# Performance work log

Hardware: AMD Instinct MI355X
Metric: run time of the kernel (lower is better)

The kernel has to match this reference:

```python
import jax, jax.numpy as jnp
import numpy as np

N_NODES = 50000
N_EDGES = 800000
NODE_DIM = 64
EDGE_DIM = 32
OUT_FEATS = 64


def setup_inputs() -> dict:
    key = jax.random.key(0)
    k1, k2, k3, k4, k5, k6, k7 = jax.random.split(key, 7)
    node_features = jax.random.normal(k1, (N_NODES, NODE_DIM), dtype=jnp.float32)
    edge_features = jax.random.normal(k2, (N_EDGES, EDGE_DIM), dtype=jnp.float32)
    src = jax.random.randint(k3, (N_EDGES,), 0, N_NODES, dtype=jnp.int32)
    dst = jax.random.randint(k4, (N_EDGES,), 0, N_NODES, dtype=jnp.int32)
    in_dim = 2 * NODE_DIM + EDGE_DIM  # concat([e_ft, h_src, h_dst])
    w_group = jax.random.normal(k5, (in_dim,), dtype=jnp.float32) * 0.05
    w_srcattn = jax.random.normal(k6, (NODE_DIM + EDGE_DIM,), dtype=jnp.float32) * 0.05
    w_lin = jax.random.normal(k7, (in_dim, OUT_FEATS), dtype=jnp.float32) * 0.05
    return {"node_features": node_features, "edge_features": edge_features,
            "src": src, "dst": dst,
            "w_group": w_group, "w_srcattn": w_srcattn, "w_lin": w_lin}


def _segment_softmax(scores, seg, num_segments):
    # numerically-stable softmax of per-edge scalar scores within each segment
    m = jax.ops.segment_max(scores, seg, num_segments=num_segments)
    e = jnp.exp(scores - m[seg])
    s = jax.ops.segment_sum(e, seg, num_segments=num_segments)
    return e / s[seg]


def reference(node_features, edge_features, src, dst, w_group, w_srcattn, w_lin):
    h = node_features              # [N, node_dim]
    e_ft = edge_features           # [E, edge_dim]
    h_src = h[src]                 # [E, node_dim]
    h_dst = h[dst]                 # [E, node_dim]

    # --- group_apply_edges(group_by='src'): edge attention over out-edges of each src ---
    z2 = jnp.concatenate([e_ft, h_src, h_dst], axis=1)      # [E, edge_dim + 2*node_dim]
    a = z2 @ w_group                                        # [E]
    gamma = _segment_softmax(a, src, N_NODES)               # softmax over edges sharing src
    e_weighted = gamma[:, None] * e_ft                      # [E, edge_dim]

    # --- gnn_msg: msg = concat([h_src, e_weighted]) ---
    msg = jnp.concatenate([h_src, e_weighted], axis=1)      # [E, node_dim + edge_dim]

    # --- gnn_reduce: attention softmax over mailbox (edges sharing dst), weighted sum ---
    s = msg @ w_srcattn                                     # [E]
    alpha = _segment_softmax(s, dst, N_NODES)
    accum = jax.ops.segment_sum(alpha[:, None] * msg, dst, num_segments=N_NODES)  # [N, node_dim+edge_dim]

    # --- node_update: linear(concat([h, accum])) + relu ---
    h_cat = jnp.concatenate([h, accum], axis=1)             # [N, 2*node_dim + edge_dim]
    out = jax.nn.relu(h_cat @ w_lin)                        # [N, out_feats]
    return out
```

## Files before the change

### kernel.cpp

```cpp
#include <hip/hip_runtime.h>

#define NN 50000
#define NE 800000
#define NEB 1563
#define NHB 3125
#define NTILES 3125

typedef __attribute__((ext_vector_type(8))) short bf16x8;
typedef __attribute__((ext_vector_type(4))) short s16x4;
typedef __attribute__((ext_vector_type(4))) float f32x4;
typedef __attribute__((ext_vector_type(4))) int   i32x4;

static __device__ __forceinline__ short f2bf(float f) {
    unsigned int u = __float_as_uint(f);
    u += 0x7FFFu + ((u >> 16) & 1u);
    return (short)(u >> 16);
}

__global__ __launch_bounds__(256) void k_pre(
    const float* __restrict__ h, const int* __restrict__ dst,
    const float* __restrict__ wg, const float* __restrict__ wa,
    int* __restrict__ cnt, int* __restrict__ rank,
    float* __restrict__ p1, float* __restrict__ pd, float* __restrict__ dpf,
    short* __restrict__ hb)
{
    int tid = threadIdx.x;
    if (blockIdx.x < NEB) {
        int e0 = blockIdx.x * 512 + tid;
        if (e0 >= NE) return;
        int e1 = e0 + 256;
        bool v1 = e1 < NE;
        int d0 = dst[e0];
        int d1 = dst[v1 ? e1 : 0];
        int r0 = atomicAdd(&cnt[d0], 1);
        int r1 = v1 ? atomicAdd(&cnt[d1], 1) : 0;
        rank[e0] = r0;
        if (v1) rank[e1] = r1;
        return;
    }
    __shared__ float4 ls[16], ld[16], lt[16];
    if (tid < 16)      ls[tid]      = ((const float4*)wg)[8 + tid];
    else if (tid < 32) ld[tid - 16] = ((const float4*)wg)[8 + tid];
    else if (tid < 48) lt[tid - 32] = ((const float4*)wa)[tid - 32];
    __syncthreads();
    int n = (blockIdx.x - NEB) * 16 + (tid >> 4);
    if (n >= NN) return;
    int l16 = tid & 15;
    float4 v = ((const float4*)(h + (size_t)n * 64))[l16];
    s16x4 hv;
    hv[0] = f2bf(v.x); hv[1] = f2bf(v.y); hv[2] = f2bf(v.z); hv[3] = f2bf(v.w);
    *(s16x4*)(hb + (size_t)n * 160 + l16 * 4) = hv;
    float4 w1 = ls[l16], w2 = ld[l16], w3 = lt[l16];
    float s1 = v.x*w1.x + v.y*w1.y + v.z*w1.z + v.w*w1.w;
    float s2 = v.x*w2.x + v.y*w2.y + v.z*w2.z + v.w*w2.w;
    float s3 = v.x*w3.x + v.y*w3.y + v.z*w3.z + v.w*w3.w;
    #pragma unroll
    for (int m = 8; m; m >>= 1) {
        s1 += __shfl_xor(s1, m);
        s2 += __shfl_xor(s2, m);
        s3 += __shfl_xor(s3, m);
    }
    if (l16 == 0) { p1[n] = s1; pd[n] = s2; dpf[2 * n + 1] = s3; }
}

__global__ __launch_bounds__(256) void k_assign(
    const int* __restrict__ cnt, int* __restrict__ off, int* __restrict__ gtotal)
{
    int n = blockIdx.x * 256 + threadIdx.x;
    int lane = threadIdx.x & 63;
    int c = (n < NN) ? cnt[n] : 0;
    int pre = c;
    #pragma unroll
    for (int d = 1; d < 64; d <<= 1) {
        int v = __shfl_up(pre, d);
        if (lane >= d) pre += v;
    }
    int base = 0;
    if (lane == 63) base = atomicAdd(gtotal, pre);
    base = __shfl(base, 63);
    if (n < NN) off[n] = base + pre - c;
}

__global__ __launch_bounds__(256) void k_edge(
    const float* __restrict__ ef, const int* __restrict__ src,
    const int* __restrict__ dst, const int* __restrict__ rank,
    const float* __restrict__ wg, const float* __restrict__ wa,
    const float* __restrict__ p1, const float* __restrict__ pd,
    float* __restrict__ dpf, const int* __restrict__ off,
    i32x4* __restrict__ recA)
{
    __shared__ float4 lwe[8], lae[8];
    int tid = threadIdx.x;
    if (tid < 8)       lwe[tid]     = ((const float4*)wg)[tid];
    else if (tid < 16) lae[tid - 8] = ((const float4*)wa)[tid - 8 + 16];
    __syncthreads();
    int e0 = blockIdx.x * 512 + tid;
    if (e0 >= NE) return;
    int e1 = e0 + 256;
    bool v1 = e1 < NE;
    int e1c = v1 ? e1 : 0;
    int s0 = src[e0], d0 = dst[e0], k0 = rank[e0];
    int s1 = src[e1c], d1 = dst[e1c], k1 = rank[e1c];
    float p1a = p1[s0], pda = pd[d0];
    float p1b = p1[s1], pdb = pd[d1];
    int o0 = off[d0], o1 = off[d1];
    const float4* ea = (const float4*)ef + (unsigned)e0 * 8u;
    const float4* eb = (const float4*)ef + (unsigned)e1c * 8u;
    float a0 = 0.f, u0 = 0.f, a1 = 0.f, u1 = 0.f;
    #pragma unroll
    for (int q = 0; q < 8; ++q) {
        float4 x = ea[q], y = eb[q];
        float4 w = lwe[q], w2 = lae[q];
        a0 += x.x*w.x  + x.y*w.y  + x.z*w.z  + x.w*w.w;
        u0 += x.x*w2.x + x.y*w2.y + x.z*w2.z + x.w*w2.w;
        a1 += y.x*w.x  + y.y*w.y  + y.z*w.z  + y.w*w.w;
        u1 += y.x*w2.x + y.y*w2.y + y.z*w2.z + y.w*w2.w;
    }
    float ev0 = __expf(a0 + p1a + pda);
    float ev1 = __expf(a1 + p1b + pdb);
    atomicAdd(&dpf[2 * s0], ev0);
    if (v1) atomicAdd(&dpf[2 * s1], ev1);
    i32x4 rc0 = (i32x4){s0, e0, __float_as_int(ev0), __float_as_int(u0)};
    __builtin_nontemporal_store(rc0, recA + (o0 + k0));
    if (v1) {
        i32x4 rc1 = (i32x4){s1, e1, __float_as_int(ev1), __float_as_int(u1)};
        __builtin_nontemporal_store(rc1, recA + (o1 + k1));
    }
}

__global__ __launch_bounds__(256) void k_reduce(
    const float* __restrict__ h, const float* __restrict__ ef,
    const int* __restrict__ cnt, const int* __restrict__ off,
    const float2* __restrict__ dp, const i32x4* __restrict__ recA,
    short* __restrict__ hb)
{
    int n = blockIdx.x * 4 + (threadIdx.x >> 6);
    if (n >= NN) return;
    int lane = threadIdx.x & 63;
    bool up = lane >= 32;
    int l5 = lane & 31;
    int deg = cnt[n], base = off[n];
    const i32x4* rp = recA + base;
    float acch = 0.f, acce = 0.f, den = 0.f;
    int j = 0;
    for (; j + 8 <= deg; j += 8) {
        i32x4 r[8];
        #pragma unroll
        for (int t = 0; t < 8; ++t) r[t] = rp[j + t];
        float2 dv[8];
        #pragma unroll
        for (int t = 0; t < 8; ++t) dv[t] = dp[r[t][0]];
        float hv[8];
        #pragma unroll
        for (int t = 0; t < 8; ++t) hv[t] = h[((unsigned)r[t][0] << 6) + lane];
        float efv[4];
        #pragma unroll
        for (int t = 0; t < 4; ++t) {
            int e = up ? r[2*t+1][1] : r[2*t][1];
            efv[t] = ef[((unsigned)e << 5) + l5];
        }
        float g[8], s[8];
        #pragma unroll
        for (int t = 0; t < 8; ++t) {
            g[t] = __int_as_float(r[t][2]) * __builtin_amdgcn_rcpf(dv[t].x);
            s[t] = __expf(dv[t].y + g[t] * __int_as_float(r[t][3]));
            den  += s[t];
            acch += s[t] * hv[t];
        }
        #pragma unroll
        for (int t = 0; t < 4; ++t) {
            float w = up ? s[2*t+1]*g[2*t+1] : s[2*t]*g[2*t];
            acce += w * efv[t];
        }
    }
    if (j + 4 <= deg) {
        i32x4 r[4];
        #pragma unroll
        for (int t = 0; t < 4; ++t) r[t] = rp[j + t];
        float2 dv[4];
        #pragma unroll
        for (int t = 0; t < 4; ++t) dv[t] = dp[r[t][0]];
        float hv[4];
        #pragma unroll
        for (int t = 0; t < 4; ++t) hv[t] = h[((unsigned)r[t][0] << 6) + lane];
        float efv[2];
        #pragma unroll
        for (int t = 0; t < 2; ++t) {
            int e = up ? r[2*t+1][1] : r[2*t][1];
            efv[t] = ef[((unsigned)e << 5) + l5];
        }
        float g[4], s[4];
        #pragma unroll
        for (int t = 0; t < 4; ++t) {
            g[t] = __int_as_float(r[t][2]) * __builtin_amdgcn_rcpf(dv[t].x);
            s[t] = __expf(dv[t].y + g[t] * __int_as_float(r[t][3]));
            den  += s[t];
            acch += s[t] * hv[t];
        }
        #pragma unroll
        for (int t = 0; t < 2; ++t) {
            float w = up ? s[2*t+1]*g[2*t+1] : s[2*t]*g[2*t];
            acce += w * efv[t];
        }
        j += 4;
    }
    for (; j < deg; ++j) {
        i32x4 r = rp[j];
        float2 dt = dp[r[0]];
        float g = __int_as_float(r[2]) * __builtin_amdgcn_rcpf(dt.x);
        float s = __expf(dt.y + g * __int_as_float(r[3]));
        den += s;
        acch += s * h[((unsigned)r[0] << 6) + lane];
        if (!up) acce += s * g * ef[((unsigned)r[1] << 5) + l5];
    }
    acce += __shfl_xor(acce, 32);
    float inv = (deg > 0) ? __builtin_amdgcn_rcpf(den) : 0.f;
    size_t hbase = (size_t)n * 160;
    hb[hbase + 64 + lane] = f2bf(acch * inv);
    if (!up) hb[hbase + 128 + l5] = f2bf(acce * inv);
}

__global__ __launch_bounds__(256) void k_node_update(
    const short* __restrict__ hb, const float* __restrict__ wl_g,
    float* __restrict__ out)
{
    int lane = threadIdx.x & 63;
    int col  = lane & 15;
    int quad = lane >> 4;
    int tile = blockIdx.x * 4 + (threadIdx.x >> 6);
    if (tile >= NTILES) return;

    bf16x8 bfr[5][4];
    #pragma unroll
    for (int kc = 0; kc < 5; ++kc)
        #pragma unroll
        for (int nt = 0; nt < 4; ++nt) {
            #pragma unroll
            for (int j = 0; j < 8; ++j) {
                int k = kc * 32 + quad * 8 + j;
                bfr[kc][nt][j] = f2bf(wl_g[k * 64 + nt * 16 + col]);
            }
        }

    int n = tile * 16 + col;
    f32x4 acc[4];
    #pragma unroll
    for (int nt = 0; nt < 4; ++nt) acc[nt] = (f32x4){0.f, 0.f, 0.f, 0.f};

    const short* hrow = hb + (size_t)n * 160 + quad * 8;
    #pragma unroll
    for (int kc = 0; kc < 5; ++kc) {
        bf16x8 af = *(const bf16x8*)(hrow + kc * 32);
        #pragma unroll
        for (int nt = 0; nt < 4; ++nt)
            acc[nt] = __builtin_amdgcn_mfma_f32_16x16x32_bf16(
                af, bfr[kc][nt], acc[nt], 0, 0, 0);
    }

    #pragma unroll
    for (int nt = 0; nt < 4; ++nt) {
        #pragma unroll
        for (int r = 0; r < 4; ++r) {
            int node = tile * 16 + quad * 4 + r;
            out[(size_t)node * 64 + nt * 16 + col] = fmaxf(acc[nt][r], 0.f);
        }
    }
}

extern "C" void kernel_launch(void* const* d_in, const int* in_sizes, int n_in,
                              void* d_out, int out_size, void* d_ws, size_t ws_size,
                              hipStream_t stream)
{
    const float* h   = (const float*)d_in[0];
    const float* ef  = (const float*)d_in[1];
    const int*   src = (const int*)d_in[2];
    const int*   dst = (const int*)d_in[3];
    const float* wg  = (const float*)d_in[4];
    const float* wa  = (const float*)d_in[5];
    const float* wl  = (const float*)d_in[6];
    float* out = (float*)d_out;

    float* ws = (float*)d_ws;
    float*  dpf    = ws;
    int*    cnt    = (int*)(ws + 2 * NN);
    int*    gtotal = (int*)(ws + 3 * NN);
    int*    off    = (int*)(ws + 3 * NN + 16);
    float*  p1     = ws + 4 * NN + 16;
    float*  pd     = ws + 5 * NN + 16;
    i32x4*  recA   = (i32x4*)(ws + 6 * NN + 16);
    int*    rank   = (int*)(ws + 6 * NN + 16 + 4 * NE);
    short*  hb     = (short*)(ws + 6 * NN + 16 + 5 * NE);

    hipMemsetAsync(d_ws, 0, (size_t)(3 * NN + 16) * sizeof(float), stream);

    k_pre<<<NEB + NHB, 256, 0, stream>>>(h, dst, wg, wa, cnt, rank, p1, pd, dpf, hb);
    k_assign<<<(NN + 255) / 256, 256, 0, stream>>>(cnt, off, gtotal);
    k_edge<<<NEB, 256, 0, stream>>>(ef, src, dst, rank, wg, wa, p1, pd, dpf,
                                    off, recA);
    k_reduce<<<(NN + 3) / 4, 256, 0, stream>>>(h, ef, cnt, off, (const float2*)dpf,
                                               recA, hb);
    k_node_update<<<782, 256, 0, stream>>>(hb, wl, out);
}
```

Before: 356.3 us.

## Replace scattered 16B edge records with int index list plus per-edge float2 data

The edge kernel now writes a coalesced per-edge float2 (exp score, attention projection) indexed by edge id, and scatters only a 4-byte edge index into the dst-sorted list instead of a 16-byte record. The reduce kernel gathers src and recB through that index, which adds an extra level of indirection. The histogram and node projection are split into separate kernels, each edge thread handles one edge, and pd and off are packed into one int2 array. The aim is to cut scattered write traffic in the edge pass, at the cost of more dependent random reads in the reduce pass.

```diff
diff --git a/kernel.cpp b/kernel.cpp
--- a/kernel.cpp
+++ b/kernel.cpp
@@ -2,14 +2,13 @@
 
 #define NN 50000
 #define NE 800000
-#define NEB 1563
+#define NEB 3125
 #define NHB 3125
 #define NTILES 3125
 
 typedef __attribute__((ext_vector_type(8))) short bf16x8;
 typedef __attribute__((ext_vector_type(4))) short s16x4;
 typedef __attribute__((ext_vector_type(4))) float f32x4;
-typedef __attribute__((ext_vector_type(4))) int   i32x4;
 
 static __device__ __forceinline__ short f2bf(float f) {
     unsigned int u = __float_as_uint(f);
@@ -17,33 +16,25 @@
     return (short)(u >> 16);
 }
 
-__global__ __launch_bounds__(256) void k_pre(
-    const float* __restrict__ h, const int* __restrict__ dst,
-    const float* __restrict__ wg, const float* __restrict__ wa,
-    int* __restrict__ cnt, int* __restrict__ rank,
-    float* __restrict__ p1, float* __restrict__ pd, float* __restrict__ dpf,
-    short* __restrict__ hb)
-{
+__global__ __launch_bounds__(256) void k_hist(
+    const int* __restrict__ dst, int* __restrict__ cnt, int* __restrict__ rank)
+{
+    int e = blockIdx.x * 256 + threadIdx.x;
+    if (e < NE) rank[e] = atomicAdd(&cnt[dst[e]], 1);
+}
+
+__global__ __launch_bounds__(256) void k_proj(
+    const float* __restrict__ h, const float* __restrict__ wg,
+    const float* __restrict__ wa, float* __restrict__ p1,
+    int2* __restrict__ pdo, float* __restrict__ dpf, short* __restrict__ hb)
+{
+    __shared__ float4 ls[16], ld[16], lt[16];
     int tid = threadIdx.x;
-    if (blockIdx.x < NEB) {
-        int e0 = blockIdx.x * 512 + tid;
-        if (e0 >= NE) return;
-        int e1 = e0 + 256;
-        bool v1 = e1 < NE;
-        int d0 = dst[e0];
-        int d1 = dst[v1 ? e1 : 0];
-        int r0 = atomicAdd(&cnt[d0], 1);
-        int r1 = v1 ? atomicAdd(&cnt[d1], 1) : 0;
-        rank[e0] = r0;
-        if (v1) rank[e1] = r1;
-        return;
-    }
-    __shared__ float4 ls[16], ld[16], lt[16];
     if (tid < 16)      ls[tid]      = ((const float4*)wg)[8 + tid];
     else if (tid < 32) ld[tid - 16] = ((const float4*)wg)[8 + tid];
     else if (tid < 48) lt[tid - 32] = ((const float4*)wa)[tid - 32];
     __syncthreads();
-    int n = (blockIdx.x - NEB) * 16 + (tid >> 4);
+    int n = blockIdx.x * 16 + (tid >> 4);
     if (n >= NN) return;
     int l16 = tid & 15;
     float4 v = ((const float4*)(h + (size_t)n * 64))[l16];
@@ -60,11 +51,15 @@
         s2 += __shfl_xor(s2, m);
         s3 += __shfl_xor(s3, m);
     }
-    if (l16 == 0) { p1[n] = s1; pd[n] = s2; dpf[2 * n + 1] = s3; }
+    if (l16 == 0) {
+        p1[n] = s1;
+        pdo[n].x = __float_as_int(s2);
+        dpf[2 * n + 1] = s3;
+    }
 }
 
 __global__ __launch_bounds__(256) void k_assign(
-    const int* __restrict__ cnt, int* __restrict__ off, int* __restrict__ gtotal)
+    const int* __restrict__ cnt, int2* __restrict__ pdo, int* __restrict__ gtotal)
 {
     int n = blockIdx.x * 256 + threadIdx.x;
     int lane = threadIdx.x & 63;
@@ -78,60 +73,48 @@
     int base = 0;
     if (lane == 63) base = atomicAdd(gtotal, pre);
     base = __shfl(base, 63);
-    if (n < NN) off[n] = base + pre - c;
+    if (n < NN) pdo[n].y = base + pre - c;
 }
 
 __global__ __launch_bounds__(256) void k_edge(
     const float* __restrict__ ef, const int* __restrict__ src,
     const int* __restrict__ dst, const int* __restrict__ rank,
     const float* __restrict__ wg, const float* __restrict__ wa,
-    const float* __restrict__ p1, const float* __restrict__ pd,
-    float* __restrict__ dpf, const int* __restrict__ off,
-    i32x4* __restrict__ recA)
+    const float* __restrict__ p1, const int2* __restrict__ pdo,
+    float* __restrict__ dpf, int* __restrict__ eidx,
+    float2* __restrict__ recB)
 {
     __shared__ float4 lwe[8], lae[8];
     int tid = threadIdx.x;
     if (tid < 8)       lwe[tid]     = ((const float4*)wg)[tid];
     else if (tid < 16) lae[tid - 8] = ((const float4*)wa)[tid - 8 + 16];
     __syncthreads();
-    int e0 = blockIdx.x * 512 + tid;
-    if (e0 >= NE) return;
-    int e1 = e0 + 256;
-    bool v1 = e1 < NE;
-    int e1c = v1 ? e1 : 0;
-    int s0 = src[e0], d0 = dst[e0], k0 = rank[e0];
-    int s1 = src[e1c], d1 = dst[e1c], k1 = rank[e1c];
-    float p1a = p1[s0], pda = pd[d0];
-    float p1b = p1[s1], pdb = pd[d1];
-    int o0 = off[d0], o1 = off[d1];
-    const float4* ea = (const float4*)ef + (unsigned)e0 * 8u;
-    const float4* eb = (const float4*)ef + (unsigned)e1c * 8u;
-    float a0 = 0.f, u0 = 0.f, a1 = 0.f, u1 = 0.f;
+    int e = blockIdx.x * 256 + tid;
+    if (e >= NE) return;
+    int s = src[e], d = dst[e], rk = rank[e];
+    float p1v = p1[s];
+    int2 pv = pdo[d];
+    float pdv = __int_as_float(pv.x);
+    int pos = pv.y + rk;
+    const float4* e4 = (const float4*)(ef + (size_t)e * 32);
+    float a = 0.f, u = 0.f;
     #pragma unroll
     for (int q = 0; q < 8; ++q) {
-        float4 x = ea[q], y = eb[q];
-        float4 w = lwe[q], w2 = lae[q];
-        a0 += x.x*w.x  + x.y*w.y  + x.z*w.z  + x.w*w.w;
-        u0 += x.x*w2.x + x.y*w2.y + x.z*w2.z + x.w*w2.w;
-        a1 += y.x*w.x  + y.y*w.y  + y.z*w.z  + y.w*w.w;
-        u1 += y.x*w2.x + y.y*w2.y + y.z*w2.z + y.w*w2.w;
-    }
-    float ev0 = __expf(a0 + p1a + pda);
-    float ev1 = __expf(a1 + p1b + pdb);
-    atomicAdd(&dpf[2 * s0], ev0);
-    if (v1) atomicAdd(&dpf[2 * s1], ev1);
-    i32x4 rc0 = (i32x4){s0, e0, __float_as_int(ev0), __float_as_int(u0)};
-    __builtin_nontemporal_store(rc0, recA + (o0 + k0));
-    if (v1) {
-        i32x4 rc1 = (i32x4){s1, e1, __float_as_int(ev1), __float_as_int(u1)};
-        __builtin_nontemporal_store(rc1, recA + (o1 + k1));
-    }
+        float4 v = e4[q], w = lwe[q], w2 = lae[q];
+        a += v.x*w.x  + v.y*w.y  + v.z*w.z  + v.w*w.w;
+        u += v.x*w2.x + v.y*w2.y + v.z*w2.z + v.w*w2.w;
+    }
+    float ev = __expf(a + p1v + pdv);
+    atomicAdd(&dpf[2 * s], ev);
+    recB[e] = make_float2(ev, u);
+    eidx[pos] = e;
 }
 
 __global__ __launch_bounds__(256) void k_reduce(
     const float* __restrict__ h, const float* __restrict__ ef,
-    const int* __restrict__ cnt, const int* __restrict__ off,
-    const float2* __restrict__ dp, const i32x4* __restrict__ recA,
+    const int* __restrict__ src, const int* __restrict__ cnt,
+    const int2* __restrict__ pdo, const float2* __restrict__ dp,
+    const int* __restrict__ eidx, const float2* __restrict__ recB,
     short* __restrict__ hb)
 {
     int n = blockIdx.x * 4 + (threadIdx.x >> 6);
@@ -139,31 +122,34 @@
     int lane = threadIdx.x & 63;
     bool up = lane >= 32;
     int l5 = lane & 31;
-    int deg = cnt[n], base = off[n];
-    const i32x4* rp = recA + base;
+    int deg = cnt[n], base = pdo[n].y;
+    const int* ep = eidx + base;
     float acch = 0.f, acce = 0.f, den = 0.f;
     int j = 0;
     for (; j + 8 <= deg; j += 8) {
-        i32x4 r[8];
-        #pragma unroll
-        for (int t = 0; t < 8; ++t) r[t] = rp[j + t];
-        float2 dv[8];
-        #pragma unroll
-        for (int t = 0; t < 8; ++t) dv[t] = dp[r[t][0]];
-        float hv[8];
-        #pragma unroll
-        for (int t = 0; t < 8; ++t) hv[t] = h[((unsigned)r[t][0] << 6) + lane];
+        int e[8];
+        #pragma unroll
+        for (int t = 0; t < 8; ++t) e[t] = ep[j + t];
+        float2 rb[8]; int sv[8];
+        #pragma unroll
+        for (int t = 0; t < 8; ++t) { rb[t] = recB[e[t]]; sv[t] = src[e[t]]; }
+        float2 dv[8]; float hv[8];
+        #pragma unroll
+        for (int t = 0; t < 8; ++t) {
+            dv[t] = dp[sv[t]];
+            hv[t] = h[((unsigned)sv[t] << 6) + lane];
+        }
         float efv[4];
         #pragma unroll
         for (int t = 0; t < 4; ++t) {
-            int e = up ? r[2*t+1][1] : r[2*t][1];
-            efv[t] = ef[((unsigned)e << 5) + l5];
+            int ee = up ? e[2*t+1] : e[2*t];
+            efv[t] = ef[((unsigned)ee << 5) + l5];
         }
         float g[8], s[8];
         #pragma unroll
         for (int t = 0; t < 8; ++t) {
-            g[t] = __int_as_float(r[t][2]) * __builtin_amdgcn_rcpf(dv[t].x);
-            s[t] = __expf(dv[t].y + g[t] * __int_as_float(r[t][3]));
+            g[t] = rb[t].x * __builtin_amdgcn_rcpf(dv[t].x);
+            s[t] = __expf(dv[t].y + g[t] * rb[t].y);
             den  += s[t];
             acch += s[t] * hv[t];
         }
@@ -174,26 +160,29 @@
         }
     }
     if (j + 4 <= deg) {
-        i32x4 r[4];
-        #pragma unroll
-        for (int t = 0; t < 4; ++t) r[t] = rp[j + t];
-        float2 dv[4];
-        #pragma unroll
-        for (int t = 0; t < 4; ++t) dv[t] = dp[r[t][0]];
-        float hv[4];
-        #pragma unroll
-        for (int t = 0; t < 4; ++t) hv[t] = h[((unsigned)r[t][0] << 6) + lane];
+        int e[4];
+        #pragma unroll
+        for (int t = 0; t < 4; ++t) e[t] = ep[j + t];
+        float2 rb[4]; int sv[4];
+        #pragma unroll
+        for (int t = 0; t < 4; ++t) { rb[t] = recB[e[t]]; sv[t] = src[e[t]]; }
+        float2 dv[4]; float hv[4];
+        #pragma unroll
+        for (int t = 0; t < 4; ++t) {
+            dv[t] = dp[sv[t]];
+            hv[t] = h[((unsigned)sv[t] << 6) + lane];
+        }
         float efv[2];
         #pragma unroll
         for (int t = 0; t < 2; ++t) {
-            int e = up ? r[2*t+1][1] : r[2*t][1];
-            efv[t] = ef[((unsigned)e << 5) + l5];
+            int ee = up ? e[2*t+1] : e[2*t];
+            efv[t] = ef[((unsigned)ee << 5) + l5];
         }
         float g[4], s[4];
         #pragma unroll
         for (int t = 0; t < 4; ++t) {
-            g[t] = __int_as_float(r[t][2]) * __builtin_amdgcn_rcpf(dv[t].x);
-            s[t] = __expf(dv[t].y + g[t] * __int_as_float(r[t][3]));
+            g[t] = rb[t].x * __builtin_amdgcn_rcpf(dv[t].x);
+            s[t] = __expf(dv[t].y + g[t] * rb[t].y);
             den  += s[t];
             acch += s[t] * hv[t];
         }
@@ -205,13 +194,15 @@
         j += 4;
     }
     for (; j < deg; ++j) {
-        i32x4 r = rp[j];
-        float2 dt = dp[r[0]];
-        float g = __int_as_float(r[2]) * __builtin_amdgcn_rcpf(dt.x);
-        float s = __expf(dt.y + g * __int_as_float(r[3]));
-        den += s;
-        acch += s * h[((unsigned)r[0] << 6) + lane];
-        if (!up) acce += s * g * ef[((unsigned)r[1] << 5) + l5];
+        int e = ep[j];
+        float2 rb = recB[e];
+        int s0 = src[e];
+        float2 dt = dp[s0];
+        float g = rb.x * __builtin_amdgcn_rcpf(dt.x);
+        float sx = __expf(dt.y + g * rb.y);
+        den += sx;
+        acch += sx * h[((unsigned)s0 << 6) + lane];
+        if (!up) acce += sx * g * ef[((unsigned)e << 5) + l5];
     }
     acce += __shfl_xor(acce, 32);
     float inv = (deg > 0) ? __builtin_amdgcn_rcpf(den) : 0.f;
@@ -280,24 +271,25 @@
     const float* wl  = (const float*)d_in[6];
     float* out = (float*)d_out;
 
-    float* ws = (float*)d_ws;
+    float*  ws     = (float*)d_ws;
     float*  dpf    = ws;
     int*    cnt    = (int*)(ws + 2 * NN);
     int*    gtotal = (int*)(ws + 3 * NN);
-    int*    off    = (int*)(ws + 3 * NN + 16);
-    float*  p1     = ws + 4 * NN + 16;
-    float*  pd     = ws + 5 * NN + 16;
-    i32x4*  recA   = (i32x4*)(ws + 6 * NN + 16);
-    int*    rank   = (int*)(ws + 6 * NN + 16 + 4 * NE);
-    short*  hb     = (short*)(ws + 6 * NN + 16 + 5 * NE);
+    int2*   pdo    = (int2*)(ws + 3 * NN + 16);
+    float*  p1     = ws + 5 * NN + 16;
+    int*    rank   = (int*)(ws + 6 * NN + 16);
+    int*    eidx   = (int*)(ws + 6 * NN + 16 + NE);
+    float2* recB   = (float2*)(ws + 6 * NN + 16 + 2 * NE);
+    short*  hb     = (short*)(ws + 6 * NN + 16 + 4 * NE);
 
     hipMemsetAsync(d_ws, 0, (size_t)(3 * NN + 16) * sizeof(float), stream);
 
-    k_pre<<<NEB + NHB, 256, 0, stream>>>(h, dst, wg, wa, cnt, rank, p1, pd, dpf, hb);
-    k_assign<<<(NN + 255) / 256, 256, 0, stream>>>(cnt, off, gtotal);
-    k_edge<<<NEB, 256, 0, stream>>>(ef, src, dst, rank, wg, wa, p1, pd, dpf,
-                                    off, recA);
-    k_reduce<<<(NN + 3) / 4, 256, 0, stream>>>(h, ef, cnt, off, (const float2*)dpf,
-                                               recA, hb);
+    k_hist<<<NEB, 256, 0, stream>>>(dst, cnt, rank);
+    k_proj<<<NHB, 256, 0, stream>>>(h, wg, wa, p1, pdo, dpf, hb);
+    k_assign<<<(NN + 255) / 256, 256, 0, stream>>>(cnt, pdo, gtotal);
+    k_edge<<<NEB, 256, 0, stream>>>(ef, src, dst, rank, wg, wa, p1, pdo,
+                                    dpf, eidx, recB);
+    k_reduce<<<(NN + 3) / 4, 256, 0, stream>>>(h, ef, src, cnt, pdo,
+                                               (const float2*)dpf, eidx, recB, hb);
     k_node_update<<<782, 256, 0, stream>>>(hb, wl, out);
 }
```

After: 352.7 us. About the same (-1.0%).
